# Performance work log

Measured on AMD Instinct MI355X. Metric: run time of the kernel, lower is better.

Reference implementation:

```python
import jax, jax.numpy as jnp
import numpy as np

K_SCOPE = 25.0
K_ENV = 100.0
K_LABEL_4 = 1.5
WIN = int(K_SCOPE) + 2
N = 65536
H = W = 4096


def setup_inputs() -> dict:
    key = jax.random.key(0)
    k1, k2, k3, k4 = jax.random.split(key, 4)
    # positions well inside the map so windows stay (mostly) in bounds
    first_frame = jax.random.uniform(k1, (N, 2), minval=64.0, maxval=H - 64.0)
    current_step = jax.random.normal(k2, (N, 2)) * 5.0
    current_vel = jax.random.normal(k3, (N, 2))
    semantic_map = jax.random.randint(k4, (H, W), 0, 6).astype(jnp.int32)
    F0 = jnp.zeros((N, 2), jnp.float32)
    return {"current_step": current_step, "first_frame": first_frame,
            "current_vel": current_vel, "semantic_map": semantic_map, "F0": F0}


def reference(current_step, first_frame, current_vel, semantic_map, F0):
    Hm, Wm = semantic_map.shape
    ori = current_step + first_frame                      # [N,2]
    scope = ori + jnp.sign(current_vel) * K_SCOPE
    a0 = jnp.floor(ori).astype(jnp.int32)                 # (r0,c0)
    a1 = jnp.floor(scope).astype(jnp.int32)               # (r1,c1)
    r0, c0 = a0[:, 0], a0[:, 1]
    r1, c1 = a1[:, 0], a1[:, 1]
    rmin, rmax = jnp.minimum(r0, r1), jnp.maximum(r0, r1)
    cmin, cmax = jnp.minimum(c0, c1), jnp.maximum(c0, c1)
    deg_r = r0 == r1
    deg_c = c0 == c1

    lr = jnp.arange(WIN)
    lc = jnp.arange(WIN)
    rows = rmin[:, None] + lr[None, :]
    cols = cmin[:, None] + lc[None, :]
    rin = (rows >= 0) & (rows < Hm)
    cin = (cols >= 0) & (cols < Wm)
    # gathered per-agent windows anchored at the region's min corner
    win = semantic_map[jnp.clip(rows, 0, Hm - 1)[:, :, None],
                       jnp.clip(cols, 0, Wm - 1)[:, None, :]]

    # region mask: degenerate axis -> single line at local index 0; else half-open extent
    mr = jnp.where(deg_r[:, None], lr[None, :] == 0, lr[None, :] < (rmax - rmin)[:, None])
    mc = jnp.where(deg_c[:, None], lc[None, :] == 0, lc[None, :] < (cmax - cmin)[:, None])
    both_deg = deg_r & deg_c
    mask = (mr & rin)[:, :, None] & (mc & cin)[:, None, :] & (~both_deg)[:, None, None]

    lr_f = lr.astype(jnp.float32)
    lc_f = lc.astype(jnp.float32)

    def force_for_label(label, weight, plus_one_row):
        match = (mask & (win == label)).astype(jnp.float32)
        cnt = jnp.sum(match, axis=(1, 2))                     # [N]
        denom = jnp.maximum(cnt, 1.0)
        mean_r = jnp.einsum('nrc,r->n', match, lr_f) / denom  # local-coord centroid
        mean_c = jnp.einsum('nrc,c->n', match, lc_f) / denom

        def safe(d):
            return jnp.where(d == 0, 1.0, d)

        # Case A: same row, cols differ (1D horizontal slice)
        disA = jnp.where(c0 < c1, mean_c, K_SCOPE - mean_c)
        dirA = jnp.where((c0 < c1)[:, None], jnp.array([0.0, -1.0]), jnp.array([0.0, 1.0]))
        FA = (weight * K_ENV / safe(disA))[:, None] * dirA
        FA = jnp.where((disA != 0)[:, None], FA, 0.0)

        # Case B: same col, rows differ (1D vertical slice); label-5 quirk adds +1
        disB = jnp.where(r0 < r1, mean_r + plus_one_row, K_SCOPE - mean_r)
        dirB = jnp.where((r0 < r1)[:, None], jnp.array([-1.0, 0.0]), jnp.array([1.0, 0.0]))
        FB = (weight * K_ENV / safe(disB))[:, None] * dirB
        FB = jnp.where((disB != 0)[:, None], FB, 0.0)

        # Case C: full 2D region, force from the corner matching travel direction
        corner = jnp.stack([jnp.where(r0 < r1, 0.0, K_SCOPE),
                            jnp.where(c0 < c1, 0.0, K_SCOPE)], axis=1)   # [N,2]
        obstacle = jnp.stack([mean_r, mean_c], axis=1)
        d = obstacle - corner
        disC = jnp.sqrt(jnp.sum(d * d, axis=1))
        FC = -(weight * K_ENV) * d / (safe(disC) ** 2)[:, None]
        FC = jnp.where((disC != 0)[:, None], FC, 0.0)

        F = jnp.where((deg_r & ~deg_c)[:, None], FA,
                      jnp.where((~deg_r & deg_c)[:, None], FB, FC))
        active = (cnt > 0) & (~both_deg)
        return jnp.where(active[:, None], F, 0.0)

    F2 = jnp.zeros_like(F0)
    F2 = F2 + force_for_label(5, 1.0, 1.0)        # label 5: +1 row-distance quirk
    F2 = F2 + force_for_label(3, 1.0, 0.0)        # label 3
    F2 = F2 + force_for_label(4, K_LABEL_4, 0.0)  # label 4, scaled by k_label_4
    return F2
```

## Files before the change

### kernel.cpp

```cpp
#include <hip/hip_runtime.h>
#include <math.h>

#define HM 4096
#define WM 4096
#define TGRID 32
#define NTILES (TGRID*TGRID)
#define CAP 80
#define POISON 0xAAAAAAAAu
#define SLOTS (NTILES*CAP)
#define SBLOCKS (SLOTS/16)
#define OBLOCKS 64


#define BYTESUM(x) ((int)(((x) * 0x01010101u) >> 24))
#define KSUM(W) ((int)(((W) >> 8) & 0xFFu) + 2 * (int)(((W) >> 16) & 0xFFu) + 3 * (int)((W) >> 24))
__device__ __forceinline__ int bytesum_safe(unsigned x) {
    unsigned t = (x & 0x00FF00FFu) + ((x >> 8) & 0x00FF00FFu);
    return (int)((t + (t >> 16)) & 0xFFFFu);
}

struct AgentGeom {
    int r0, c0, r1, c1;
    int rmin, cmin;
    int nr, nc;
    bool deg_r, deg_c, both;
};

__device__ __forceinline__ AgentGeom agent_geom(const float* __restrict__ cstep,
                                                const float* __restrict__ fframe,
                                                const float* __restrict__ cvel, int n)
{
    AgentGeom g;
    const float ori_r = cstep[2*n+0] + fframe[2*n+0];
    const float ori_c = cstep[2*n+1] + fframe[2*n+1];
    const float vr = cvel[2*n+0], vc = cvel[2*n+1];
    const float sgr = (vr > 0.f) ? 1.f : ((vr < 0.f) ? -1.f : 0.f);
    const float sgc = (vc > 0.f) ? 1.f : ((vc < 0.f) ? -1.f : 0.f);
    g.r0 = (int)floorf(ori_r);
    g.c0 = (int)floorf(ori_c);
    g.r1 = (int)floorf(ori_r + sgr * 25.0f);
    g.c1 = (int)floorf(ori_c + sgc * 25.0f);
    g.rmin = min(g.r0, g.r1);
    g.cmin = min(g.c0, g.c1);
    g.deg_r = (g.r0 == g.r1);
    g.deg_c = (g.c0 == g.c1);
    g.both  = g.deg_r && g.deg_c;
    g.nr = g.deg_r ? 1 : min(max(g.r0, g.r1) - g.rmin, 27);
    g.nc = g.deg_c ? 1 : min(max(g.c0, g.c1) - g.cmin, 27);
    return g;
}

__device__ __forceinline__ void force_from_counts(const AgentGeom& g,
    const int cnts[3], const int srs[3], const int scs[3], float& Fr, float& Fc)
{
    const float wts[3] = {1.0f, 1.0f, 1.5f};
    const float p1s[3] = {1.0f, 0.0f, 0.0f};
    Fr = 0.0f; Fc = 0.0f;
    #pragma unroll
    for (int i = 0; i < 3; ++i) {
        const float denom  = fmaxf((float)cnts[i], 1.0f);
        const float mean_r = (float)srs[i] / denom;
        const float mean_c = (float)scs[i] / denom;
        float fr, fc;
        if (g.deg_r && !g.deg_c) {
            const float disA = (g.c0 < g.c1) ? mean_c : (25.0f - mean_c);
            const float mag  = (disA != 0.0f) ? (wts[i] * 100.0f / disA) : 0.0f;
            fr = 0.0f;
            fc = (g.c0 < g.c1) ? -mag : mag;
        } else if (!g.deg_r && g.deg_c) {
            const float disB = (g.r0 < g.r1) ? (mean_r + p1s[i]) : (25.0f - mean_r);
            const float mag  = (disB != 0.0f) ? (wts[i] * 100.0f / disB) : 0.0f;
            fr = (g.r0 < g.r1) ? -mag : mag;
            fc = 0.0f;
        } else {
            const float crn_r = (g.r0 < g.r1) ? 0.0f : 25.0f;
            const float crn_c = (g.c0 < g.c1) ? 0.0f : 25.0f;
            const float dr = mean_r - crn_r;
            const float dc = mean_c - crn_c;
            const float disC = sqrtf(dr * dr + dc * dc);
            if (disC != 0.0f) {
                const float s = -(wts[i] * 100.0f) / (disC * disC);
                fr = s * dr; fc = s * dc;
            } else { fr = 0.0f; fc = 0.0f; }
        }
        if (cnts[i] > 0 && !g.both) { Fr += fr; Fc += fc; }
    }
}

__device__ __forceinline__ int agent_tile(const float* __restrict__ cstep,
                                          const float* __restrict__ fframe, int n)
{
    const float orr = cstep[2*n+0] + fframe[2*n+0];
    const float occ = cstep[2*n+1] + fframe[2*n+1];
    const int r = min(max((int)floorf(orr), 0), HM - 1);
    const int c = min(max((int)floorf(occ), 0), WM - 1);
    return ((r >> 7) << 5) | (c >> 7);
}

__global__ __launch_bounds__(256) void nsp_place(
    const float* __restrict__ cstep, const float* __restrict__ fframe,
    unsigned* __restrict__ wsw, int N)
{
    const int n = blockIdx.x * blockDim.x + threadIdx.x;
    if (n >= N) return;
    unsigned* tcnt  = wsw;
    unsigned* ocnt  = wsw + NTILES;
    int*      olist = (int*)(ocnt + 1);
    int*      slot  = olist + N;
    const int t = agent_tile(cstep, fframe, n);
    const unsigned rank = atomicAdd(&tcnt[t], 1u) - POISON;
    if (rank < CAP) {
        slot[t * CAP + rank] = n;
    } else {
        const unsigned op = atomicAdd(ocnt, 1u) - POISON;
        olist[op] = n;
    }
}

__device__ __forceinline__ void gather_body4(
    const float* __restrict__ cstep, const float* __restrict__ fframe,
    const float* __restrict__ cvel, const int* __restrict__ smap,
    float* __restrict__ out, int n, bool live, int lane)
{
    const int l4  = lane & 15;
    const AgentGeom g = agent_geom(cstep, fframe, cvel, n);

    const int cg  = l4 & 7;
    const int rho = l4 >> 3;
    const int a   = g.cmin & ~3;
    const int d   = g.cmin - a;

    unsigned B = 0;
    #pragma unroll
    for (int k = 0; k < 4; ++k) {
        const int wc  = cg * 4 + k - d;
        const int col = a + cg * 4 + k;
        const bool bad = ((unsigned)wc >= (unsigned)g.nc) ||
                         ((unsigned)col >= (unsigned)WM);
        B |= bad ? (0xFFu << (8 * k)) : 0u;
    }

    const int T      = (g.nr + 1) >> 1;
    const int t_lane = (rho < g.nr) ? ((g.nr - rho + 1) >> 1) : 0;
    int Tw = max(T, __shfl_xor(T, 16));
    Tw = max(Tw, __shfl_xor(Tw, 32));

    const bool fastl = (g.rmin >= 0) && (g.rmin + 28 <= HM) &&
                       (a >= 0) && (a + 32 <= WM);
    const bool fastw = __all(fastl ? 1 : 0);

    unsigned W5 = 0, S5 = 0, W3 = 0, S3 = 0, W4 = 0, S4 = 0;
    const unsigned k01 = 0x01010101u;

    if (fastw) {
        const int* p = smap + (size_t)(g.rmin + rho) * WM + a + cg * 4;
        #pragma unroll 2
        for (int j = 0; j < Tw; ++j) {
            const int4 v = *reinterpret_cast<const int4*>(p);
            p += 2 * WM;
            unsigned y = __builtin_amdgcn_perm((unsigned)v.y, (unsigned)v.x, 0x0C0C0400u)
                       | __builtin_amdgcn_perm((unsigned)v.w, (unsigned)v.z, 0x04000C0Cu);
            y |= B;
            y = (j < t_lane) ? y : 0xFFFFFFFFu;
            const unsigned b1 = y >> 1, b2 = y >> 2;
            const unsigned m5 = ( y & ~b1 &  b2) & k01;
            const unsigned m3 = ( y &  b1 & ~b2) & k01;
            const unsigned m4 = (~y & ~b1 &  b2) & k01;
            W5 += m5; S5 += W5;
            W3 += m3; S3 += W3;
            W4 += m4; S4 += W4;
        }
    } else {
        for (int j = 0; j < Tw; ++j) {
            const int rrow = g.rmin + rho + 2 * j;
            const int rcl  = min(max(rrow, 0), HM - 1);
            unsigned y = 0;
            #pragma unroll
            for (int k = 0; k < 4; ++k) {
                const int col  = a + cg * 4 + k;
                const int colc = min(max(col, 0), WM - 1);
                y |= ((unsigned)smap[(size_t)rcl * WM + colc]) << (8 * k);
            }
            y |= B;
            const bool rok = (j < t_lane) && ((unsigned)rrow < (unsigned)HM);
            y = rok ? y : 0xFFFFFFFFu;
            const unsigned b1 = y >> 1, b2 = y >> 2;
            const unsigned m5 = ( y & ~b1 &  b2) & k01;
            const unsigned m3 = ( y &  b1 & ~b2) & k01;
            const unsigned m4 = (~y & ~b1 &  b2) & k01;
            W5 += m5; S5 += W5;
            W3 += m3; S3 += W3;
            W4 += m4; S4 += W4;
        }
    }

    const int c5 = BYTESUM(W5), c3 = BYTESUM(W3), c4 = BYTESUM(W4);
    const int rs5 = rho * c5 + 2 * (Tw * c5 - bytesum_safe(S5));
    const int rs3 = rho * c3 + 2 * (Tw * c3 - bytesum_safe(S3));
    const int rs4 = rho * c4 + 2 * (Tw * c4 - bytesum_safe(S4));
    const int cbase = cg * 4 - d;
    const int cs5  = cbase * c5 + KSUM(W5);
    const int cs3  = cbase * c3 + KSUM(W3);
    const int cs4v = cbase * c4 + KSUM(W4);

    unsigned q5 = (unsigned)c5 | ((unsigned)rs5 << 10);
    unsigned q3 = (unsigned)c3 | ((unsigned)rs3 << 10);
    unsigned q4 = (unsigned)c4 | ((unsigned)rs4 << 10);
    unsigned scp = (unsigned)cs5 | ((unsigned)cs3 << 15);
    int      sc4 = cs4v;

    #pragma unroll
    for (int o = 1; o <= 8; o <<= 1) {
        q5  += __shfl_xor(q5, o);
        q3  += __shfl_xor(q3, o);
        q4  += __shfl_xor(q4, o);
        scp += __shfl_xor(scp, o);
        sc4 += __shfl_xor(sc4, o);
    }

    if (l4 == 0 && live) {
        const int cnts[3] = {(int)(q5 & 1023u), (int)(q3 & 1023u), (int)(q4 & 1023u)};
        const int srs[3]  = {(int)(q5 >> 10),   (int)(q3 >> 10),   (int)(q4 >> 10)};
        const int scs[3]  = {(int)(scp & 0x7FFFu), (int)(scp >> 15), sc4};
        float Fr, Fc;
        force_from_counts(g, cnts, srs, scs, Fr, Fc);
        out[2*n+0] = Fr;
        out[2*n+1] = Fc;
    }
}

__global__ __launch_bounds__(256) void nsp_gather_s4(
    const float* __restrict__ cstep, const float* __restrict__ fframe,
    const float* __restrict__ cvel, const int* __restrict__ smap,
    const unsigned* __restrict__ wsw, float* __restrict__ out, int N)
{
    const unsigned* tcnt  = wsw;
    const unsigned* ocnt  = wsw + NTILES;
    const int*      olist = (const int*)(ocnt + 1);
    const int*      slot  = olist + N;

    const int lane = threadIdx.x & 63;
    const int sub  = lane >> 4;
    const int widx = threadIdx.x >> 6;

    if (blockIdx.x < SBLOCKS) {
        const int cpx = SBLOCKS >> 3;
        const int bid = ((int)blockIdx.x & 7) * cpx + ((int)blockIdx.x >> 3);
        const int sid = bid * 16 + widx * 4 + sub;
        const int t   = sid / CAP;
        const int s   = sid - t * CAP;
        const unsigned cnt = min(tcnt[t] - POISON, (unsigned)CAP);
        const bool live = (unsigned)s < cnt;
        if (__ballot(live ? 1 : 0) == 0ull) return;
        const int n = live ? slot[t * CAP + s] : 0;
        gather_body4(cstep, fframe, cvel, smap, out, n, live, lane);
    } else {
        const int ow = ((int)blockIdx.x - SBLOCKS) * 4 + widx;
        const int OW = OBLOCKS * 4;
        unsigned oc = ocnt[0] - POISON;
        if (oc > (unsigned)N) oc = 0;
        for (int base = ow * 4; base < (int)oc; base += OW * 4) {
            const int i = base + sub;
            const bool live = i < (int)oc;
            const int n = live ? olist[i] : 0;
            gather_body4(cstep, fframe, cvel, smap, out, n, live, lane);
        }
    }
}

__global__ __launch_bounds__(256) void nsp_gather_flat(
    const float* __restrict__ cstep, const float* __restrict__ fframe,
    const float* __restrict__ cvel, const int* __restrict__ smap,
    float* __restrict__ out, int N)
{
    const int wave = (blockIdx.x * blockDim.x + threadIdx.x) >> 6;
    const int lane = threadIdx.x & 63;
    const int sub  = lane >> 4;
    const int idx  = wave * 4 + sub;
    const bool live = (idx < N);
    gather_body4(cstep, fframe, cvel, smap, out, live ? idx : 0, live, lane);
}

extern "C" void kernel_launch(void* const* d_in, const int* in_sizes, int n_in,
                              void* d_out, int out_size, void* d_ws, size_t ws_size,
                              hipStream_t stream) {
    const float* cstep  = (const float*)d_in[0];
    const float* fframe = (const float*)d_in[1];
    const float* cvel   = (const float*)d_in[2];
    const int*   smap   = (const int*)d_in[3];
    float* out = (float*)d_out;

    const int N = in_sizes[0] / 2;
    const size_t need = (size_t)(NTILES + 1 + N + SLOTS) * sizeof(int);

    if (d_ws != nullptr && ws_size >= need) {
        unsigned* wsw = (unsigned*)d_ws;
        hipLaunchKernelGGL(nsp_place, dim3((N + 255) / 256), dim3(256), 0, stream,
                           cstep, fframe, wsw, N);
        hipLaunchKernelGGL(nsp_gather_s4, dim3(SBLOCKS + OBLOCKS), dim3(256), 0, stream,
                           cstep, fframe, cvel, smap, wsw, out, N);
    } else {
        const int waves  = (N + 3) / 4;
        const int blocks = (waves + 3) / 4;
        hipLaunchKernelGGL(nsp_gather_flat, dim3(blocks), dim3(256), 0, stream,
                           cstep, fframe, cvel, smap, out, N);
    }
}
```

Measured before the change: 138.4 us.

## Pack semantic map into per-label bitmasks and gather windows with popcounts

A new prep kernel reads the whole int32 semantic map on every call. It packs it into per-label bitmasks: one bit per cell for labels 5, 3 and 4, as 32-column words stored in a uint4 per row chunk. Agent tile placement is fused into the same launch. The gather kernel then reads two uint4 words per window row instead of 27 int32 values. It computes the counts, row sums and column sums with masked popcounts. This cuts gather memory traffic and ALU work, at the cost of a full streaming pass over the 64 MB map and an extra 8 MB of workspace. Label classification looks only at the low three bits of the low byte of each cell, so any map value outside 0..7 would alias onto another label.

New measurement: 131.6 us. 4.9% less time.

```diff
diff --git a/kernel.cpp b/kernel.cpp
--- a/kernel.cpp
+++ b/kernel.cpp
@@ -10,6 +10,7 @@
 #define SLOTS (NTILES*CAP)
 #define SBLOCKS (SLOTS/16)
 #define OBLOCKS 64
+#define BM_U32  (4096*128*4)
 
 
 #define BYTESUM(x) ((int)(((x) * 0x01010101u) >> 24))
@@ -97,23 +98,172 @@
     return ((r >> 7) << 5) | (c >> 7);
 }
 
-__global__ __launch_bounds__(256) void nsp_place(
+__global__ __launch_bounds__(256) void nsp_prep_place(
+    const int* __restrict__ smap, const float* __restrict__ cstep,
+    const float* __restrict__ fframe, unsigned* __restrict__ wsw, int N)
+{
+    const int tid = blockIdx.x * blockDim.x + threadIdx.x;
+
+    {
+        const int row = tid >> 7;
+        const int ch  = tid & 127;
+        const int* src = smap + (size_t)row * WM + ch * 32;
+        const unsigned k01 = 0x01010101u;
+        unsigned n5 = 0, n3 = 0, n4 = 0;
+        #pragma unroll
+        for (int wI = 0; wI < 8; ++wI) {
+            const int4 v = *reinterpret_cast<const int4*>(src + wI * 4);
+            const unsigned y =
+                __builtin_amdgcn_perm((unsigned)v.y, (unsigned)v.x, 0x0C0C0400u) |
+                __builtin_amdgcn_perm((unsigned)v.w, (unsigned)v.z, 0x04000C0Cu);
+            const unsigned b1 = y >> 1, b2 = y >> 2;
+            const unsigned m5 = ( y & ~b1 &  b2) & k01;
+            const unsigned m3 = ( y &  b1 & ~b2) & k01;
+            const unsigned m4 = (~y & ~b1 &  b2) & k01;
+            n5 |= (((m5 * 0x01020408u) >> 24) & 0xFu) << (4 * wI);
+            n3 |= (((m3 * 0x01020408u) >> 24) & 0xFu) << (4 * wI);
+            n4 |= (((m4 * 0x01020408u) >> 24) & 0xFu) << (4 * wI);
+        }
+        reinterpret_cast<uint4*>(wsw)[tid] = make_uint4(n5, n3, n4, 0u);
+    }
+
+    if (tid < N) {
+        unsigned* tcnt  = wsw + BM_U32;
+        unsigned* ocnt  = tcnt + NTILES;
+        int*      olist = (int*)(ocnt + 1);
+        int*      slot  = olist + N;
+        const int t = agent_tile(cstep, fframe, tid);
+        const unsigned rank = atomicAdd(&tcnt[t], 1u) - POISON;
+        if (rank < CAP) {
+            slot[t * CAP + rank] = tid;
+        } else {
+            const unsigned op = atomicAdd(ocnt, 1u) - POISON;
+            olist[op] = tid;
+        }
+    }
+}
+
+__device__ __forceinline__ void gather_body_bm(
     const float* __restrict__ cstep, const float* __restrict__ fframe,
-    unsigned* __restrict__ wsw, int N)
-{
-    const int n = blockIdx.x * blockDim.x + threadIdx.x;
-    if (n >= N) return;
-    unsigned* tcnt  = wsw;
-    unsigned* ocnt  = wsw + NTILES;
-    int*      olist = (int*)(ocnt + 1);
-    int*      slot  = olist + N;
-    const int t = agent_tile(cstep, fframe, n);
-    const unsigned rank = atomicAdd(&tcnt[t], 1u) - POISON;
-    if (rank < CAP) {
-        slot[t * CAP + rank] = n;
+    const float* __restrict__ cvel, const uint4* __restrict__ bm4,
+    float* __restrict__ out, int n, bool live, int lane)
+{
+    const int l4 = lane & 15;
+    const AgentGeom g = agent_geom(cstep, fframe, cvel, n);
+
+    unsigned colmask = (1u << g.nc) - 1u;
+    if (g.cmin < 0) {
+        const int cut = -g.cmin;
+        colmask &= (cut >= 32) ? 0u : ~((1u << cut) - 1u);
+    }
+    {
+        const int hcut = WM - g.cmin;
+        if (hcut < 32) colmask &= (hcut <= 0) ? 0u : ((1u << hcut) - 1u);
+    }
+    const unsigned sh = (unsigned)g.cmin & 31u;
+    const int b   = g.cmin >> 5;
+    const int bc  = min(max(b, 0), 127);
+    const int bc2 = min(max(b + 1, 0), 127);
+
+    int c5 = 0, sr5 = 0, cs5 = 0;
+    int c3 = 0, sr3 = 0, cs3 = 0;
+    int c4 = 0, sr4 = 0, cs4 = 0;
+
+    #pragma unroll
+    for (int s = 0; s < 2; ++s) {
+        const int rb  = l4 + 16 * s;
+        const int row = g.rmin + rb;
+        const bool rv = (rb < g.nr) && ((unsigned)row < (unsigned)HM);
+        const int rowc = min(max(row, 0), HM - 1);
+        const uint4 lo = bm4[(size_t)rowc * 128 + bc];
+        const uint4 hi = bm4[(size_t)rowc * 128 + bc2];
+        const unsigned cm = rv ? colmask : 0u;
+
+        const unsigned long long q5w = ((unsigned long long)hi.x << 32) | lo.x;
+        const unsigned long long q3w = ((unsigned long long)hi.y << 32) | lo.y;
+        const unsigned long long q4w = ((unsigned long long)hi.z << 32) | lo.z;
+        const unsigned v5 = (unsigned)(q5w >> sh) & cm;
+        const unsigned v3 = (unsigned)(q3w >> sh) & cm;
+        const unsigned v4 = (unsigned)(q4w >> sh) & cm;
+
+        int t;
+        t = __popc(v5); c5 += t; sr5 += rb * t;
+        cs5 += __popc(v5 & 0xAAAAAAAAu) + 2 * __popc(v5 & 0xCCCCCCCCu)
+             + 4 * __popc(v5 & 0xF0F0F0F0u) + 8 * __popc(v5 & 0xFF00FF00u)
+             + 16 * __popc(v5 & 0xFFFF0000u);
+        t = __popc(v3); c3 += t; sr3 += rb * t;
+        cs3 += __popc(v3 & 0xAAAAAAAAu) + 2 * __popc(v3 & 0xCCCCCCCCu)
+             + 4 * __popc(v3 & 0xF0F0F0F0u) + 8 * __popc(v3 & 0xFF00FF00u)
+             + 16 * __popc(v3 & 0xFFFF0000u);
+        t = __popc(v4); c4 += t; sr4 += rb * t;
+        cs4 += __popc(v4 & 0xAAAAAAAAu) + 2 * __popc(v4 & 0xCCCCCCCCu)
+             + 4 * __popc(v4 & 0xF0F0F0F0u) + 8 * __popc(v4 & 0xFF00FF00u)
+             + 16 * __popc(v4 & 0xFFFF0000u);
+    }
+
+    unsigned q5 = (unsigned)c5 | ((unsigned)sr5 << 10);
+    unsigned q3 = (unsigned)c3 | ((unsigned)sr3 << 10);
+    unsigned q4 = (unsigned)c4 | ((unsigned)sr4 << 10);
+    unsigned scp = (unsigned)cs5 | ((unsigned)cs3 << 15);
+    int      sc4 = cs4;
+
+    #pragma unroll
+    for (int o = 1; o <= 8; o <<= 1) {
+        q5  += __shfl_xor(q5, o);
+        q3  += __shfl_xor(q3, o);
+        q4  += __shfl_xor(q4, o);
+        scp += __shfl_xor(scp, o);
+        sc4 += __shfl_xor(sc4, o);
+    }
+
+    if (l4 == 0 && live) {
+        const int cnts[3] = {(int)(q5 & 1023u), (int)(q3 & 1023u), (int)(q4 & 1023u)};
+        const int srs[3]  = {(int)(q5 >> 10),   (int)(q3 >> 10),   (int)(q4 >> 10)};
+        const int scs[3]  = {(int)(scp & 0x7FFFu), (int)(scp >> 15), sc4};
+        float Fr, Fc;
+        force_from_counts(g, cnts, srs, scs, Fr, Fc);
+        out[2*n+0] = Fr;
+        out[2*n+1] = Fc;
+    }
+}
+
+__global__ __launch_bounds__(256) void nsp_gather_bm(
+    const float* __restrict__ cstep, const float* __restrict__ fframe,
+    const float* __restrict__ cvel, const unsigned* __restrict__ wsw,
+    float* __restrict__ out, int N)
+{
+    const uint4*    bm4   = reinterpret_cast<const uint4*>(wsw);
+    const unsigned* tcnt  = wsw + BM_U32;
+    const unsigned* ocnt  = tcnt + NTILES;
+    const int*      olist = (const int*)(ocnt + 1);
+    const int*      slot  = olist + N;
+
+    const int lane = threadIdx.x & 63;
+    const int sub  = lane >> 4;
+    const int widx = threadIdx.x >> 6;
+
+    if (blockIdx.x < SBLOCKS) {
+        const int cpx = SBLOCKS >> 3;
+        const int bid = ((int)blockIdx.x & 7) * cpx + ((int)blockIdx.x >> 3);
+        const int sid = bid * 16 + widx * 4 + sub;
+        const int t   = sid / CAP;
+        const int s   = sid - t * CAP;
+        const unsigned cnt = min(tcnt[t] - POISON, (unsigned)CAP);
+        const bool live = (unsigned)s < cnt;
+        if (__ballot(live ? 1 : 0) == 0ull) return;
+        const int n = live ? slot[t * CAP + s] : 0;
+        gather_body_bm(cstep, fframe, cvel, bm4, out, n, live, lane);
     } else {
-        const unsigned op = atomicAdd(ocnt, 1u) - POISON;
-        olist[op] = n;
+        const int ow = ((int)blockIdx.x - SBLOCKS) * 4 + widx;
+        const int OW = OBLOCKS * 4;
+        unsigned oc = ocnt[0] - POISON;
+        if (oc > (unsigned)N) oc = 0;
+        for (int base = ow * 4; base < (int)oc; base += OW * 4) {
+            const int i = base + sub;
+            const bool live = i < (int)oc;
+            const int n = live ? olist[i] : 0;
+            gather_body_bm(cstep, fframe, cvel, bm4, out, n, live, lane);
+        }
     }
 }
 
@@ -229,45 +379,6 @@
     }
 }
 
-__global__ __launch_bounds__(256) void nsp_gather_s4(
-    const float* __restrict__ cstep, const float* __restrict__ fframe,
-    const float* __restrict__ cvel, const int* __restrict__ smap,
-    const unsigned* __restrict__ wsw, float* __restrict__ out, int N)
-{
-    const unsigned* tcnt  = wsw;
-    const unsigned* ocnt  = wsw + NTILES;
-    const int*      olist = (const int*)(ocnt + 1);
-    const int*      slot  = olist + N;
-
-    const int lane = threadIdx.x & 63;
-    const int sub  = lane >> 4;
-    const int widx = threadIdx.x >> 6;
-
-    if (blockIdx.x < SBLOCKS) {
-        const int cpx = SBLOCKS >> 3;
-        const int bid = ((int)blockIdx.x & 7) * cpx + ((int)blockIdx.x >> 3);
-        const int sid = bid * 16 + widx * 4 + sub;
-        const int t   = sid / CAP;
-        const int s   = sid - t * CAP;
-        const unsigned cnt = min(tcnt[t] - POISON, (unsigned)CAP);
-        const bool live = (unsigned)s < cnt;
-        if (__ballot(live ? 1 : 0) == 0ull) return;
-        const int n = live ? slot[t * CAP + s] : 0;
-        gather_body4(cstep, fframe, cvel, smap, out, n, live, lane);
-    } else {
-        const int ow = ((int)blockIdx.x - SBLOCKS) * 4 + widx;
-        const int OW = OBLOCKS * 4;
-        unsigned oc = ocnt[0] - POISON;
-        if (oc > (unsigned)N) oc = 0;
-        for (int base = ow * 4; base < (int)oc; base += OW * 4) {
-            const int i = base + sub;
-            const bool live = i < (int)oc;
-            const int n = live ? olist[i] : 0;
-            gather_body4(cstep, fframe, cvel, smap, out, n, live, lane);
-        }
-    }
-}
-
 __global__ __launch_bounds__(256) void nsp_gather_flat(
     const float* __restrict__ cstep, const float* __restrict__ fframe,
     const float* __restrict__ cvel, const int* __restrict__ smap,
@@ -291,14 +402,14 @@
     float* out = (float*)d_out;
 
     const int N = in_sizes[0] / 2;
-    const size_t need = (size_t)(NTILES + 1 + N + SLOTS) * sizeof(int);
+    const size_t need = ((size_t)BM_U32 + NTILES + 1 + N + SLOTS) * sizeof(int);
 
     if (d_ws != nullptr && ws_size >= need) {
         unsigned* wsw = (unsigned*)d_ws;
-        hipLaunchKernelGGL(nsp_place, dim3((N + 255) / 256), dim3(256), 0, stream,
-                           cstep, fframe, wsw, N);
-        hipLaunchKernelGGL(nsp_gather_s4, dim3(SBLOCKS + OBLOCKS), dim3(256), 0, stream,
-                           cstep, fframe, cvel, smap, wsw, out, N);
+        hipLaunchKernelGGL(nsp_prep_place, dim3((HM * WM / 32) / 256), dim3(256), 0,
+                           stream, smap, cstep, fframe, wsw, N);
+        hipLaunchKernelGGL(nsp_gather_bm, dim3(SBLOCKS + OBLOCKS), dim3(256), 0,
+                           stream, cstep, fframe, cvel, wsw, out, N);
     } else {
         const int waves  = (N + 3) / 4;
         const int blocks = (waves + 3) / 4;
```
